# Performance work log

Measured on AMD Instinct MI355X. Metric: run time of the kernel, lower is better.

Reference implementation:

```python
import jax, jax.numpy as jnp
import numpy as np

D_K = 64  # per-head key dim, used for 1/sqrt(d_k) scaling

def setup_inputs() -> dict:
    key = jax.random.key(0)
    ks = jax.random.split(key, 5)
    B, S, D, H, DK, DV = 4, 2048, 1024, 16, 64, 64
    # xavier_normal-ish scale for [D, DK] weights
    w_std = float(np.sqrt(2.0 / (D + DK)))
    return {
        "x":  jax.random.normal(ks[0], (B, S, D), dtype=jnp.float32),
        "W_Q": jax.random.normal(ks[1], (H, D, DK), dtype=jnp.float32) * w_std,
        "W_K": jax.random.normal(ks[2], (H, D, DK), dtype=jnp.float32) * w_std,
        "W_V": jax.random.normal(ks[3], (H, D, DV), dtype=jnp.float32) * w_std,
        "W_O": jax.random.normal(ks[4], (H * DV, D), dtype=jnp.float32) * float(np.sqrt(1.0 / (H * DV))),
    }

def reference(x, W_Q, W_K, W_V, W_O):
    # x: [B,S,D]; W_Q/W_K/W_V: [H,D,Dk]; W_O: [H*Dv, D]
    q = jnp.einsum("bsd,hdk->bhsk", x, W_Q)
    k = jnp.einsum("bsd,hdk->bhsk", x, W_K)
    v = jnp.einsum("bsd,hdv->bhsv", x, W_V)
    scale = 1.0 / jnp.sqrt(jnp.asarray(D_K, dtype=x.dtype))
    scores = jnp.einsum("bhsk,bhtk->bhst", q, k) * scale  # [B,H,S,S]
    weights = jax.nn.softmax(scores, axis=-1)
    out = jnp.einsum("bhst,bhtv->bhsv", weights, v)       # [B,H,S,Dv]
    B, H, S, DV = out.shape
    # concat heads in order head0..headH-1 along last dim, matching slice writes
    attn_out = jnp.transpose(out, (0, 2, 1, 3)).reshape(B, S, H * DV)
    return attn_out @ W_O
```

## Files before the change

kernel.cpp:

```cpp
#include <hip/hip_runtime.h>
#include <hip/hip_bf16.h>
#include <math.h>

#define BB 4
#define SS 2048
#define DD 1024
#define HH 16
#define DKV 64

typedef __attribute__((ext_vector_type(8))) short bf16x8;
typedef __attribute__((ext_vector_type(4))) float f32x4;
typedef __attribute__((ext_vector_type(2))) __fp16 f16x2;
typedef __attribute__((ext_vector_type(4))) __fp16 f16x4;
typedef unsigned short u16;
typedef unsigned int u32;

__device__ inline u16 f2bf(float f) {
  union { float f; u32 u; } v; v.f = f;
  u32 r = v.u + 0x7FFFu + ((v.u >> 16) & 1u);
  return (u16)(r >> 16);
}
__device__ inline u32 pack2bf(float a, float b) {
  return (u32)f2bf(a) | ((u32)f2bf(b) << 16);
}
__device__ inline u32 pack2h(float a, float b) {
  union { f16x2 h; u32 u; } c;
  c.h = __builtin_amdgcn_cvt_pkrtz(a, b);
  return c.u;
}
__device__ inline void gload16(const u16* g, u16* l) {
  __builtin_amdgcn_global_load_lds(
      (const __attribute__((address_space(1))) u32*)g,
      (__attribute__((address_space(3))) u32*)l, 16, 0, 0);
}

__global__ __launch_bounds__(256) void cvt_x(const float* __restrict__ x,
                                             u16* __restrict__ xb) {
  const long i = ((long)blockIdx.x * 256 + threadIdx.x) * 4;
  const float4 v = *(const float4*)&x[i];
  uint2 o = {pack2bf(v.x, v.y), pack2bf(v.z, v.w)};
  *(uint2*)&xb[i] = o;
}

__global__ __launch_bounds__(256) void wqkv_trans(
    const float* __restrict__ Wq, const float* __restrict__ Wk,
    const float* __restrict__ Wv, u16* __restrict__ Wt) {
  __shared__ u16 T[64][65];
  const int z = blockIdx.z;
  const int which = z >> 4, h = z & 15;
  const float* inb =
      (which == 0 ? Wq : (which == 1 ? Wk : Wv)) + (long)h * DD * DKV;
  u16* outb = Wt + (long)which * DD * DD + (long)h * DKV * DD;
  const int r0 = blockIdx.x * 64;
  const int t = threadIdx.x;
  const int r = t >> 2, cc = (t & 3) * 16;
#pragma unroll
  for (int j = 0; j < 16; j += 4) {
    const float4 v = *(const float4*)&inb[(long)(r0 + r) * DKV + cc + j];
    T[cc + j + 0][r] = f2bf(v.x);
    T[cc + j + 1][r] = f2bf(v.y);
    T[cc + j + 2][r] = f2bf(v.z);
    T[cc + j + 3][r] = f2bf(v.w);
  }
  __syncthreads();
  const int c = t >> 2, rr = (t & 3) * 16;
  u16 tmp[16];
#pragma unroll
  for (int j = 0; j < 16; ++j) tmp[j] = T[c][rr + j];
  *(uint4*)&outb[(long)c * DD + r0 + rr] = *(uint4*)&tmp[0];
  *(uint4*)&outb[(long)c * DD + r0 + rr + 8] = *(uint4*)&tmp[8];
}

__global__ __launch_bounds__(256) void wo_trans(const float* __restrict__ in,
                                                u16* __restrict__ out) {
  __shared__ u16 T[64][65];
  const int r0 = blockIdx.x * 64, c0 = blockIdx.y * 64;
  const int t = threadIdx.x;
  const int r = t >> 2, cc = (t & 3) * 16;
#pragma unroll
  for (int j = 0; j < 16; j += 4) {
    const float4 v = *(const float4*)&in[(long)(r0 + r) * DD + c0 + cc + j];
    T[cc + j + 0][r] = f2bf(v.x);
    T[cc + j + 1][r] = f2bf(v.y);
    T[cc + j + 2][r] = f2bf(v.z);
    T[cc + j + 3][r] = f2bf(v.w);
  }
  __syncthreads();
  const int c = t >> 2, rr = (t & 3) * 16;
  u16 tmp[16];
#pragma unroll
  for (int j = 0; j < 16; ++j) tmp[j] = T[c][rr + j];
  *(uint4*)&out[(long)(c0 + c) * DD + r0 + rr] = *(uint4*)&tmp[0];
  *(uint4*)&out[(long)(c0 + c) * DD + r0 + rr + 8] = *(uint4*)&tmp[8];
}

__global__ __launch_bounds__(256) void gemm_qkv(
    const u16* __restrict__ xb, const u16* __restrict__ Wt,
    u16* __restrict__ Q, u16* __restrict__ K, u16* __restrict__ Vt) {
  __shared__ u16 Xs[128][32];
  __shared__ u16 Ws[128][32];
  const int tid = threadIdx.x;
  const int wv = tid >> 6, lane = tid & 63;
  const int quad = lane >> 4, ln = lane & 15;
  const int m0 = blockIdx.x * 128, n0 = blockIdx.y * 128;
  const int mbase = (wv & 1) * 64, nbase = (wv >> 1) * 64;
  f32x4 zero = {0.f, 0.f, 0.f, 0.f};
  f32x4 acc[4][4];
#pragma unroll
  for (int a = 0; a < 4; ++a)
#pragma unroll
    for (int b = 0; b < 4; ++b) acc[a][b] = zero;
  const int srow = wv * 32 + (lane >> 2);
  const int ch = (lane & 3) * 8;
  const u16* gx0 = &xb[(long)(m0 + srow) * DD + ch];
  const u16* gx1 = &xb[(long)(m0 + srow + 16) * DD + ch];
  const u16* gw0 = &Wt[(long)(n0 + srow) * DD + ch];
  const u16* gw1 = &Wt[(long)(n0 + srow + 16) * DD + ch];
  u16* lx0 = &Xs[wv * 32][0];
  u16* lx1 = &Xs[wv * 32 + 16][0];
  u16* lw0 = &Ws[wv * 32][0];
  u16* lw1 = &Ws[wv * 32 + 16][0];
  const int which = n0 >> 10;
  if (which < 2) {
    for (int kt = 0; kt < DD; kt += 32) {
      __syncthreads();
      gload16(gx0, lx0);
      gload16(gx1, lx1);
      gload16(gw0, lw0);
      gload16(gw1, lw1);
      gx0 += 32; gx1 += 32; gw0 += 32; gw1 += 32;
      __syncthreads();
      bf16x8 a[4], b[4];
#pragma unroll
      for (int g = 0; g < 4; ++g) {
        a[g] = *(const bf16x8*)&Xs[mbase + g * 16 + ln][quad * 8];
        b[g] = *(const bf16x8*)&Ws[nbase + g * 16 + ln][quad * 8];
      }
#pragma unroll
      for (int mg = 0; mg < 4; ++mg)
#pragma unroll
        for (int ng = 0; ng < 4; ++ng)
          acc[mg][ng] = __builtin_amdgcn_mfma_f32_16x16x32_bf16(
              b[ng], a[mg], acc[mg][ng], 0, 0, 0);
    }
    const float qs = 0.18033688011112042f;
    u16* O = which == 0 ? Q : K;
    const float sc = which == 0 ? qs : 1.0f;
#pragma unroll
    for (int mg = 0; mg < 4; ++mg) {
      const int m = m0 + mbase + mg * 16 + ln;
      const int b_ = m >> 11, s_ = m & (SS - 1);
#pragma unroll
      for (int ng = 0; ng < 4; ++ng) {
        const int rem = (n0 + nbase + ng * 16 + quad * 4) & 1023;
        const int h = rem >> 6, nv = rem & 63;
        const long off = (((long)b_ * HH + h) * SS + s_) * DKV + nv;
        const f32x4 v = acc[mg][ng];
        uint2 o = {pack2bf(v[0] * sc, v[1] * sc), pack2bf(v[2] * sc, v[3] * sc)};
        *(uint2*)&O[off] = o;
      }
    }
  } else {
    for (int kt = 0; kt < DD; kt += 32) {
      __syncthreads();
      gload16(gx0, lx0);
      gload16(gx1, lx1);
      gload16(gw0, lw0);
      gload16(gw1, lw1);
      gx0 += 32; gx1 += 32; gw0 += 32; gw1 += 32;
      __syncthreads();
      bf16x8 a[4], b[4];
#pragma unroll
      for (int g = 0; g < 4; ++g) {
        a[g] = *(const bf16x8*)&Xs[mbase + g * 16 + ln][quad * 8];
        b[g] = *(const bf16x8*)&Ws[nbase + g * 16 + ln][quad * 8];
      }
#pragma unroll
      for (int mg = 0; mg < 4; ++mg)
#pragma unroll
        for (int ng = 0; ng < 4; ++ng)
          acc[mg][ng] = __builtin_amdgcn_mfma_f32_16x16x32_bf16(
              a[mg], b[ng], acc[mg][ng], 0, 0, 0);
    }
#pragma unroll
    for (int mg = 0; mg < 4; ++mg) {
      const int m = m0 + mbase + mg * 16 + quad * 4;
      const int b_ = m >> 11, s_ = m & (SS - 1);
#pragma unroll
      for (int ng = 0; ng < 4; ++ng) {
        const int rem = (n0 + nbase + ng * 16 + ln) & 1023;
        const int h = rem >> 6, nv = rem & 63;
        const f32x4 v = acc[mg][ng];
        uint2 o = {pack2h(v[0], v[1]), pack2h(v[2], v[3])};
        *(uint2*)&Vt[(((long)b_ * HH + h) * DKV + nv) * SS + s_] = o;
      }
    }
  }
}

__global__ __launch_bounds__(256) void attn_mfma(
    const u16* Qg, const u16* __restrict__ Kg, const u16* __restrict__ Vtg,
    u16* Og) {
  __shared__ u16 Ks[64][72];
  __shared__ u16 Vs[64][140];
  const int tid = threadIdx.x;
  const int wv = tid >> 6, lane = tid & 63;
  const int quad = lane >> 4, ln = lane & 15;
  const long base = (long)blockIdx.y * SS * DKV;
  const int s0 = blockIdx.x * 256;
  bf16x8 qf[4][2];
#pragma unroll
  for (int qg = 0; qg < 4; ++qg)
#pragma unroll
    for (int ks = 0; ks < 2; ++ks)
      qf[qg][ks] = *(const bf16x8*)&Qg[base +
          (long)(s0 + wv * 64 + qg * 16 + ln) * DKV + ks * 32 + quad * 8];
  f32x4 zero = {0.f, 0.f, 0.f, 0.f};
  f32x4 minus8 = {-8.f, -8.f, -8.f, -8.f};
  f32x4 of[4][4];
#pragma unroll
  for (int qg = 0; qg < 4; ++qg)
#pragma unroll
    for (int dvg = 0; dvg < 4; ++dvg) of[qg][dvg] = zero;
  float lp[4] = {0.f, 0.f, 0.f, 0.f};
  const int sr = tid >> 2, sc0 = (tid & 3) * 16;
  for (int t0 = 0; t0 < SS; t0 += 64) {
    const uint4 kv0 = *(const uint4*)&Kg[base + (long)(t0 + sr) * DKV + sc0];
    const uint4 kv1 = *(const uint4*)&Kg[base + (long)(t0 + sr) * DKV + sc0 + 8];
    const uint4 vv0 = *(const uint4*)&Vtg[base + (long)sr * SS + t0 + sc0];
    const uint4 vv1 = *(const uint4*)&Vtg[base + (long)sr * SS + t0 + sc0 + 8];
    __syncthreads();
    *(uint4*)&Ks[sr][sc0] = kv0;
    *(uint4*)&Ks[sr][sc0 + 8] = kv1;
    {
      uint2 lo0 = {vv0.x, vv0.y}, hi0 = {vv0.z, vv0.w};
      uint2 lo1 = {vv1.x, vv1.y}, hi1 = {vv1.z, vv1.w};
      *(uint2*)&Vs[sr][sc0] = lo0;
      *(uint2*)&Vs[sr][sc0 + 4] = hi0;
      *(uint2*)&Vs[sr][sc0 + 8] = lo1;
      *(uint2*)&Vs[sr][sc0 + 12] = hi1;
    }
    __syncthreads();
    f16x4 pb[4][4];
#pragma unroll
    for (int kg = 0; kg < 4; ++kg) {
      bf16x8 kf0 = *(const bf16x8*)&Ks[kg * 16 + ln][quad * 8];
      bf16x8 kf1 = *(const bf16x8*)&Ks[kg * 16 + ln][32 + quad * 8];
#pragma unroll
      for (int qg = 0; qg < 4; ++qg) {
        f32x4 st = minus8;
        st = __builtin_amdgcn_mfma_f32_16x16x32_bf16(kf0, qf[qg][0], st, 0, 0, 0);
        st = __builtin_amdgcn_mfma_f32_16x16x32_bf16(kf1, qf[qg][1], st, 0, 0, 0);
        f32x4 p;
#pragma unroll
        for (int i = 0; i < 4; ++i) p[i] = __builtin_amdgcn_exp2f(st[i]);
        lp[qg] += (p[0] + p[1]) + (p[2] + p[3]);
        const f16x2 lo = __builtin_amdgcn_cvt_pkrtz(p[0], p[1]);
        const f16x2 hi = __builtin_amdgcn_cvt_pkrtz(p[2], p[3]);
        pb[kg][qg] = __builtin_shufflevector(lo, hi, 0, 1, 2, 3);
      }
    }
#pragma unroll
    for (int dvg = 0; dvg < 4; ++dvg) {
      f16x4 vf[4];
#pragma unroll
      for (int kg = 0; kg < 4; ++kg)
        vf[kg] = *(const f16x4*)&Vs[dvg * 16 + ln][kg * 16 + quad * 4];
#pragma unroll
      for (int qg = 0; qg < 4; ++qg)
#pragma unroll
        for (int kg = 0; kg < 4; ++kg)
          of[qg][dvg] = __builtin_amdgcn_mfma_f32_16x16x16f16(
              vf[kg], pb[kg][qg], of[qg][dvg], 0, 0, 0);
    }
  }
#pragma unroll
  for (int qg = 0; qg < 4; ++qg) {
    float l = lp[qg];
    l += __shfl_xor(l, 16);
    l += __shfl_xor(l, 32);
    const float inv = 1.f / l;
    const long row = base + (long)(s0 + wv * 64 + qg * 16 + ln) * DKV;
#pragma unroll
    for (int dvg = 0; dvg < 4; ++dvg) {
      const f32x4 v = of[qg][dvg];
      uint2 o = {pack2bf(v[0] * inv, v[1] * inv), pack2bf(v[2] * inv, v[3] * inv)};
      *(uint2*)&Og[row + dvg * 16 + quad * 4] = o;
    }
  }
}

__global__ __launch_bounds__(256) void gemm_out(
    const u16* __restrict__ A, const u16* __restrict__ Wot,
    float* __restrict__ out) {
  __shared__ u16 Xs[128][32];
  __shared__ u16 Ws[128][32];
  const int tid = threadIdx.x;
  const int wv = tid >> 6, lane = tid & 63;
  const int quad = lane >> 4, ln = lane & 15;
  const int m0 = blockIdx.x * 128, n0 = blockIdx.y * 128;
  const int mbase = (wv & 1) * 64, nbase = (wv >> 1) * 64;
  f32x4 zero = {0.f, 0.f, 0.f, 0.f};
  f32x4 acc[4][4];
#pragma unroll
  for (int a = 0; a < 4; ++a)
#pragma unroll
    for (int b = 0; b < 4; ++b) acc[a][b] = zero;
  const int srow = wv * 32 + (lane >> 2);
  const int ch = (lane & 3) * 8;
  const int am0 = m0 + srow, am1 = m0 + srow + 16;
  const long ac0 = ((long)(am0 >> 11) * HH) * SS * DKV + (long)(am0 & (SS - 1)) * DKV;
  const long ac1 = ((long)(am1 >> 11) * HH) * SS * DKV + (long)(am1 & (SS - 1)) * DKV;
  const u16* gw0 = &Wot[(long)(n0 + srow) * DD + ch];
  const u16* gw1 = &Wot[(long)(n0 + srow + 16) * DD + ch];
  u16* lx0 = &Xs[wv * 32][0];
  u16* lx1 = &Xs[wv * 32 + 16][0];
  u16* lw0 = &Ws[wv * 32][0];
  u16* lw1 = &Ws[wv * 32 + 16][0];
  for (int kt = 0; kt < DD; kt += 32) {
    const long hoff = (long)(kt >> 6) * SS * DKV + (kt & 63) + ch;
    __syncthreads();
    gload16(&A[ac0 + hoff], lx0);
    gload16(&A[ac1 + hoff], lx1);
    gload16(gw0, lw0);
    gload16(gw1, lw1);
    gw0 += 32; gw1 += 32;
    __syncthreads();
    bf16x8 a[4], b[4];
#pragma unroll
    for (int g = 0; g < 4; ++g) {
      a[g] = *(const bf16x8*)&Xs[mbase + g * 16 + ln][quad * 8];
      b[g] = *(const bf16x8*)&Ws[nbase + g * 16 + ln][quad * 8];
    }
#pragma unroll
    for (int mg = 0; mg < 4; ++mg)
#pragma unroll
      for (int ng = 0; ng < 4; ++ng)
        acc[mg][ng] = __builtin_amdgcn_mfma_f32_16x16x32_bf16(
            b[ng], a[mg], acc[mg][ng], 0, 0, 0);
  }
#pragma unroll
  for (int mg = 0; mg < 4; ++mg) {
    const long row = (long)(m0 + mbase + mg * 16 + ln) * DD;
#pragma unroll
    for (int ng = 0; ng < 4; ++ng)
      *(f32x4*)&out[row + n0 + nbase + ng * 16 + quad * 4] = acc[mg][ng];
  }
}

extern "C" void kernel_launch(void* const* d_in, const int* in_sizes, int n_in,
                              void* d_out, int out_size, void* d_ws, size_t ws_size,
                              hipStream_t stream) {
  const float* x  = (const float*)d_in[0];
  const float* Wq = (const float*)d_in[1];
  const float* Wk = (const float*)d_in[2];
  const float* Wv = (const float*)d_in[3];
  const float* Wo = (const float*)d_in[4];
  float* out = (float*)d_out;
  u16* xb  = (u16*)d_ws;
  u16* Wt  = xb + (size_t)8192 * 1024;
  u16* Wot = Wt + (size_t)3072 * 1024;
  u16* Q   = Wot + (size_t)1024 * 1024;
  u16* K   = Q + (size_t)BB * HH * SS * DKV;
  u16* Vt  = K + (size_t)BB * HH * SS * DKV;
  const dim3 blk(256);
  cvt_x<<<dim3(8192), blk, 0, stream>>>(x, xb);
  wqkv_trans<<<dim3(16, 1, 48), blk, 0, stream>>>(Wq, Wk, Wv, Wt);
  wo_trans<<<dim3(16, 16), blk, 0, stream>>>(Wo, Wot);
  gemm_qkv<<<dim3(64, 24), blk, 0, stream>>>(xb, Wt, Q, K, Vt);
  attn_mfma<<<dim3(8, 64), blk, 0, stream>>>(Q, K, Vt, Q);
  gemm_out<<<dim3(64, 8), blk, 0, stream>>>(Q, Wot, out);
}
```

Measured before the change: 298.2 us.

## Shrink attention blocks to 128 threads, prefetch K/V tiles, use MFMA row-sum

The attention kernel now runs 128-thread blocks covering 128 queries each, on a grid twice as large, with launch bounds asking for two blocks per SIMD. The next K/V tile is loaded into registers while the current tile is computed, so global load latency overlaps with MFMA work. The softmax denominator comes from an extra MFMA against a ones vector rather than scalar adds and cross-lane shuffles. The costs are more registers for the prefetch buffers, halved K/V reuse per block, and a row sum taken over fp16-rounded probabilities.

```diff
diff --git a/kernel.cpp b/kernel.cpp
--- a/kernel.cpp
+++ b/kernel.cpp
@@ -198,7 +198,7 @@
   }
 }
 
-__global__ __launch_bounds__(256) void attn_mfma(
+__global__ __launch_bounds__(128, 2) void attn_mfma(
     const u16* Qg, const u16* __restrict__ Kg, const u16* __restrict__ Vtg,
     u16* Og) {
   __shared__ u16 Ks[64][72];
@@ -207,7 +207,7 @@
   const int wv = tid >> 6, lane = tid & 63;
   const int quad = lane >> 4, ln = lane & 15;
   const long base = (long)blockIdx.y * SS * DKV;
-  const int s0 = blockIdx.x * 256;
+  const int s0 = blockIdx.x * 128;
   bf16x8 qf[4][2];
 #pragma unroll
   for (int qg = 0; qg < 4; ++qg)
@@ -218,29 +218,42 @@
   f32x4 zero = {0.f, 0.f, 0.f, 0.f};
   f32x4 minus8 = {-8.f, -8.f, -8.f, -8.f};
   f32x4 of[4][4];
-#pragma unroll
-  for (int qg = 0; qg < 4; ++qg)
+  f32x4 ofl[4];
+#pragma unroll
+  for (int qg = 0; qg < 4; ++qg) {
+    ofl[qg] = zero;
 #pragma unroll
     for (int dvg = 0; dvg < 4; ++dvg) of[qg][dvg] = zero;
-  float lp[4] = {0.f, 0.f, 0.f, 0.f};
-  const int sr = tid >> 2, sc0 = (tid & 3) * 16;
+  }
+  const f16x4 ones = {(__fp16)1.f, (__fp16)1.f, (__fp16)1.f, (__fp16)1.f};
+  const int srw = tid & 63, shf = (tid >> 6) * 32;
+  const u16* kp = &Kg[base + (long)srw * DKV + shf];
+  const u16* vp = &Vtg[base + (long)srw * SS + shf];
+  uint4 kreg[4], vreg[4];
+#pragma unroll
+  for (int j = 0; j < 4; ++j) {
+    kreg[j] = *(const uint4*)(kp + 8 * j);
+    vreg[j] = *(const uint4*)(vp + 8 * j);
+  }
   for (int t0 = 0; t0 < SS; t0 += 64) {
-    const uint4 kv0 = *(const uint4*)&Kg[base + (long)(t0 + sr) * DKV + sc0];
-    const uint4 kv1 = *(const uint4*)&Kg[base + (long)(t0 + sr) * DKV + sc0 + 8];
-    const uint4 vv0 = *(const uint4*)&Vtg[base + (long)sr * SS + t0 + sc0];
-    const uint4 vv1 = *(const uint4*)&Vtg[base + (long)sr * SS + t0 + sc0 + 8];
     __syncthreads();
-    *(uint4*)&Ks[sr][sc0] = kv0;
-    *(uint4*)&Ks[sr][sc0 + 8] = kv1;
-    {
-      uint2 lo0 = {vv0.x, vv0.y}, hi0 = {vv0.z, vv0.w};
-      uint2 lo1 = {vv1.x, vv1.y}, hi1 = {vv1.z, vv1.w};
-      *(uint2*)&Vs[sr][sc0] = lo0;
-      *(uint2*)&Vs[sr][sc0 + 4] = hi0;
-      *(uint2*)&Vs[sr][sc0 + 8] = lo1;
-      *(uint2*)&Vs[sr][sc0 + 12] = hi1;
+#pragma unroll
+    for (int j = 0; j < 4; ++j) {
+      *(uint4*)&Ks[srw][shf + 8 * j] = kreg[j];
+      uint2 lo = {vreg[j].x, vreg[j].y}, hi = {vreg[j].z, vreg[j].w};
+      *(uint2*)&Vs[srw][shf + 8 * j] = lo;
+      *(uint2*)&Vs[srw][shf + 8 * j + 4] = hi;
     }
     __syncthreads();
+    if (t0 + 64 < SS) {
+      const u16* kp2 = &Kg[base + (long)(t0 + 64 + srw) * DKV + shf];
+      const u16* vp2 = &Vtg[base + (long)srw * SS + t0 + 64 + shf];
+#pragma unroll
+      for (int j = 0; j < 4; ++j) {
+        kreg[j] = *(const uint4*)(kp2 + 8 * j);
+        vreg[j] = *(const uint4*)(vp2 + 8 * j);
+      }
+    }
     f16x4 pb[4][4];
 #pragma unroll
     for (int kg = 0; kg < 4; ++kg) {
@@ -254,10 +267,11 @@
         f32x4 p;
 #pragma unroll
         for (int i = 0; i < 4; ++i) p[i] = __builtin_amdgcn_exp2f(st[i]);
-        lp[qg] += (p[0] + p[1]) + (p[2] + p[3]);
         const f16x2 lo = __builtin_amdgcn_cvt_pkrtz(p[0], p[1]);
         const f16x2 hi = __builtin_amdgcn_cvt_pkrtz(p[2], p[3]);
         pb[kg][qg] = __builtin_shufflevector(lo, hi, 0, 1, 2, 3);
+        ofl[qg] = __builtin_amdgcn_mfma_f32_16x16x16f16(
+            ones, pb[kg][qg], ofl[qg], 0, 0, 0);
       }
     }
 #pragma unroll
@@ -276,10 +290,7 @@
   }
 #pragma unroll
   for (int qg = 0; qg < 4; ++qg) {
-    float l = lp[qg];
-    l += __shfl_xor(l, 16);
-    l += __shfl_xor(l, 32);
-    const float inv = 1.f / l;
+    const float inv = 1.f / ofl[qg][0];
     const long row = base + (long)(s0 + wv * 64 + qg * 16 + ln) * DKV;
 #pragma unroll
     for (int dvg = 0; dvg < 4; ++dvg) {
@@ -368,6 +379,6 @@
   wqkv_trans<<<dim3(16, 1, 48), blk, 0, stream>>>(Wq, Wk, Wv, Wt);
   wo_trans<<<dim3(16, 16), blk, 0, stream>>>(Wo, Wot);
   gemm_qkv<<<dim3(64, 24), blk, 0, stream>>>(xb, Wt, Q, K, Vt);
-  attn_mfma<<<dim3(8, 64), blk, 0, stream>>>(Q, K, Vt, Q);
+  attn_mfma<<<dim3(16, 64), dim3(128), 0, stream>>>(Q, K, Vt, Q);
   gemm_out<<<dim3(64, 8), blk, 0, stream>>>(Q, Wot, out);
 }
```

Result: slower. 322.5 us (+8.2%).
